# Kernel tuning notes

Hardware: AMD Instinct MI355X
Metric: run time of the kernel (lower is better)

Reference implementation:

```python
import jax, jax.numpy as jnp
import numpy as np

B, S, D = 1, 2048, 1024          # batch, seq, n_embd
E, F = 16, 1024                  # n_routed_experts, moe_intermediate_size
NG, TKG, K = 4, 2, 4             # n_group, topk_group, num_experts_per_tok
NSH = 2                          # n_shared_experts
SCALE = 2.5                      # routed_scaling_factor
STD = 0.02
EPG = E // NG                    # experts per group


def setup_inputs() -> dict:
    key = jax.random.key(0)
    ks = jax.random.split(key, 8)
    return {
        "hidden_states": jax.random.normal(ks[0], (B, S, D), jnp.float32),
        "router_w": jax.random.normal(ks[1], (E, D), jnp.float32) * STD,   # gate.weight
        "bias": jnp.zeros((E,), jnp.float32),                              # e_score_correction_bias
        "gate_w": jax.random.normal(ks[2], (E, D, F), jnp.float32) * STD,  # per-expert gate_proj (transposed)
        "up_w": jax.random.normal(ks[3], (E, D, F), jnp.float32) * STD,    # per-expert up_proj
        "down_w": jax.random.normal(ks[4], (E, F, D), jnp.float32) * STD,  # per-expert down_proj
        "sh_gate_w": jax.random.normal(ks[5], (D, NSH * F), jnp.float32) * STD,
        "sh_up_w": jax.random.normal(ks[6], (D, NSH * F), jnp.float32) * STD,
        "sh_down_w": jax.random.normal(ks[7], (NSH * F, D), jnp.float32) * STD,
    }


def _route(x_flat, router_w, bias):
    # x_flat: [T, D] -> topk_idx [T, K], topk_w [T, K]
    logits = x_flat.astype(jnp.float32) @ router_w.T          # [T, E]
    scores = jax.nn.sigmoid(logits)
    s = scores + bias[None, :]                                # scores_for_choice
    sg = s.reshape(-1, NG, EPG)
    group_score = jax.lax.top_k(sg, 2)[0].sum(-1)             # sum of top-2 per group [T, NG]
    gidx = jax.lax.top_k(group_score, TKG)[1]                 # [T, TKG]
    gmask = jnp.sum(jax.nn.one_hot(gidx, NG, dtype=jnp.float32), axis=1) > 0   # [T, NG]
    emask = jnp.repeat(gmask, EPG, axis=1)                    # [T, E]
    masked = jnp.where(emask, s, -1.0)
    topk_idx = jax.lax.top_k(masked, K)[1]                    # [T, K]
    tw = jnp.take_along_axis(scores, topk_idx, axis=1)        # gather raw sigmoid scores
    tw = tw / (tw.sum(-1, keepdims=True) + 1e-20)             # norm_topk_prob
    tw = tw * SCALE
    return topk_idx, tw


def reference(hidden_states, router_w, bias, gate_w, up_w, down_w,
              sh_gate_w, sh_up_w, sh_down_w):
    x = hidden_states.reshape(-1, D)                          # [T, D]
    topk_idx, tw = _route(x, router_w, bias)
    # combine weights per (token, expert): scatter-add of topk weights
    combine = (jax.nn.one_hot(topk_idx, E, dtype=tw.dtype) * tw[..., None]).sum(1)  # [T, E]
    # per-expert SwiGLU MLPs (dense dispatch, masked combine == index_add semantics)
    h = jnp.einsum('td,edf->etf', x, gate_w)                  # [E, T, F]
    u = jnp.einsum('td,edf->etf', x, up_w)
    y = jnp.einsum('etf,efd->etd', jax.nn.silu(h) * u, down_w)  # [E, T, D]
    routed = jnp.einsum('etd,te->td', y, combine)             # weighted combine
    # shared experts
    sh = (jax.nn.silu(x @ sh_gate_w) * (x @ sh_up_w)) @ sh_down_w
    return (routed + sh).reshape(hidden_states.shape)
```

## Files before the change

kernel.cpp:

```cpp
#include <hip/hip_runtime.h>
#include <cstdint>
#include <cstddef>


#define T_TOK 2048
#define DIM   1024
#define NEXP  16
#define MAXTILES 80
#define SH_TILES 32
#define GRID_Y (MAXTILES + SH_TILES)
#define NBLK (8 * GRID_Y)
#define ABASE_SH 10240

typedef __bf16 bf16x8_t __attribute__((ext_vector_type(8)));
typedef float  f32x4_t  __attribute__((ext_vector_type(4)));
typedef unsigned short ushort8_t __attribute__((ext_vector_type(8)));
typedef unsigned short ushort4_t __attribute__((ext_vector_type(4)));

#define OFF_XB     (0UL)
#define OFF_SHGT   (4UL<<20)
#define OFF_SHUT   (8UL<<20)
#define OFF_GATET  (12UL<<20)
#define OFF_UPT    (44UL<<20)
#define OFF_DOWNT  (76UL<<20)
#define OFF_SHDT   (108UL<<20)
#define OFF_ACT    (112UL<<20)
#define OFF_YSLOT  (140UL<<20)
#define OFF_PART   (0UL)
#define OFF_CTRL   (160UL<<20)
#define CT_OFFSETS  128
#define CT_NTILES   192
#define CT_TILEEXP  256
#define CT_SLOTTOK  4096
#define CT_TKSLOT   49152
#define CT_TOPKIDX  81920
#define CT_TOPKW    114688

__device__ __forceinline__ unsigned short f2bf(float f) {
  __bf16 h = (__bf16)f;
  return __builtin_bit_cast(unsigned short, h);
}
__device__ __forceinline__ float bf2f(unsigned short u) {
  unsigned int v = ((unsigned int)u) << 16;
  return __builtin_bit_cast(float, v);
}
__device__ __forceinline__ void gld16(const void* g, void* l) {
  __builtin_amdgcn_global_load_lds(
      (const __attribute__((address_space(1))) void*)(g),
      (__attribute__((address_space(3))) void*)(l), 16, 0, 0);
}

#define VWAIT6 asm volatile("s_waitcnt vmcnt(6)" ::: "memory")
#define VWAIT4 asm volatile("s_waitcnt vmcnt(4)" ::: "memory")
#define VWAIT0 asm volatile("s_waitcnt vmcnt(0)" ::: "memory")
#define BAR { __builtin_amdgcn_s_barrier(); __builtin_amdgcn_sched_barrier(0); }

__device__ __forceinline__ void tbody(const float* __restrict__ src,
                                      unsigned short* __restrict__ dst,
                                      int R, int C) {
  __shared__ unsigned short tile[128 * 132];
  int cT = blockIdx.x * 128, rT = blockIdx.y * 128;
  int t = threadIdx.x;
  int rb = t >> 5, cb = t & 31;
  float f[4][4][4];
#pragma unroll
  for (int p = 0; p < 4; p++)
#pragma unroll
    for (int i = 0; i < 4; i++) {
      float4 v = *(const float4*)(src + (long)(rT + p * 32 + 4 * rb + i) * C + cT + 4 * cb);
      f[p][i][0] = v.x; f[p][i][1] = v.y; f[p][i][2] = v.z; f[p][i][3] = v.w;
    }
#pragma unroll
  for (int p = 0; p < 4; p++)
#pragma unroll
    for (int j = 0; j < 4; j++) {
      ushort4_t o;
      o[0] = f2bf(f[p][0][j]); o[1] = f2bf(f[p][1][j]);
      o[2] = f2bf(f[p][2][j]); o[3] = f2bf(f[p][3][j]);
      *(ushort4_t*)&tile[(4 * cb + j) * 132 + p * 32 + 4 * rb] = o;
    }
  __syncthreads();
#pragma unroll
  for (int m = 0; m < 8; m++) {
    int q = t + 256 * m;
    int c = q >> 4, r0 = (q & 15) * 8;
    ushort4_t lo = *(const ushort4_t*)&tile[c * 132 + r0];
    ushort4_t hi = *(const ushort4_t*)&tile[c * 132 + r0 + 4];
    ushort8_t w8 = {lo[0], lo[1], lo[2], lo[3], hi[0], hi[1], hi[2], hi[3]};
    *(ushort8_t*)(dst + (long)(cT + c) * R + rT + r0) = w8;
  }
}

__global__ void k_transpose(const float* __restrict__ src, unsigned short* __restrict__ dst,
                            int R, int C) {
  long b = blockIdx.z;
  tbody(src + b * (long)R * C, dst + b * (long)R * C, R, C);
}

__global__ void k_transpose3(const float* __restrict__ g, const float* __restrict__ u,
                             const float* __restrict__ d, unsigned short* __restrict__ gT,
                             unsigned short* __restrict__ uT, unsigned short* __restrict__ dT) {
  int z = blockIdx.z;
  int which = z >> 4;
  long b = z & 15;
  const float* s = (which == 0) ? g : (which == 1) ? u : d;
  unsigned short* t = (which == 0) ? gT : (which == 1) ? uT : dT;
  tbody(s + b * 1048576L, t + b * 1048576L, 1024, 1024);
}

__global__ void k_transpose_sh(const float* __restrict__ sg, const float* __restrict__ su,
                               unsigned short* __restrict__ gT, unsigned short* __restrict__ uT) {
  const float* s = blockIdx.z ? su : sg;
  unsigned short* t = blockIdx.z ? uT : gT;
  tbody(s, t, 1024, 2048);
}

__global__ __launch_bounds__(256) void k_router(
    const float* __restrict__ x, const float* __restrict__ rw,
    const float* __restrict__ bias, int* __restrict__ topk_idx,
    float* __restrict__ topk_w, unsigned short* __restrict__ xb) {
  int t = blockIdx.x, tid = threadIdx.x;
  int wv = tid >> 6, lane = tid & 63;
  float4 xv = ((const float4*)(x + (size_t)t * DIM))[tid];
  ushort4_t xo;
  xo[0] = f2bf(xv.x); xo[1] = f2bf(xv.y); xo[2] = f2bf(xv.z); xo[3] = f2bf(xv.w);
  ((ushort4_t*)(xb + (size_t)t * DIM))[tid] = xo;
  float part[NEXP];
#pragma unroll
  for (int e = 0; e < NEXP; e++) {
    float4 wr = ((const float4*)(rw + (size_t)e * DIM))[tid];
    part[e] = xv.x * wr.x + xv.y * wr.y + xv.z * wr.z + xv.w * wr.w;
  }
  __shared__ float wsum_s[4 * NEXP];
#pragma unroll
  for (int e = 0; e < NEXP; e++) {
    float v = part[e];
#pragma unroll
    for (int off = 32; off; off >>= 1) v += __shfl_xor(v, off, 64);
    if (lane == 0) wsum_s[wv * NEXP + e] = v;
  }
  __syncthreads();
  if (tid == 0) {
    float r_sc[NEXP], r_s[NEXP];
#pragma unroll
    for (int e = 0; e < NEXP; e++) {
      float logit = wsum_s[e] + wsum_s[NEXP + e] + wsum_s[2 * NEXP + e] +
                    wsum_s[3 * NEXP + e];
      float sc = 1.f / (1.f + expf(-logit));
      r_sc[e] = sc;
      r_s[e] = sc + bias[e];
    }
    float gs[4];
#pragma unroll
    for (int g = 0; g < 4; g++) {
      float m1 = -1e30f, m2 = -1e30f;
#pragma unroll
      for (int j = 0; j < 4; j++) {
        float v = r_s[g * 4 + j];
        if (v > m1) { m2 = m1; m1 = v; } else if (v > m2) m2 = v;
      }
      gs[g] = m1 + m2;
    }
    int g1 = 0;
    for (int g = 1; g < 4; g++) if (gs[g] > gs[g1]) g1 = g;
    int g2 = -1;
    for (int g = 0; g < 4; g++) { if (g == g1) continue; if (g2 < 0 || gs[g] > gs[g2]) g2 = g; }
    int taken = 0, idx[4];
    float w[4], wsum = 1e-20f;
#pragma unroll
    for (int k = 0; k < 4; k++) {
      float best = -1e30f; int bi = 0;
#pragma unroll
      for (int e2 = 0; e2 < 16; e2++) {
        if (taken & (1 << e2)) continue;
        int g = e2 >> 2;
        float v = (g == g1 || g == g2) ? r_s[e2] : -1.f;
        if (v > best) { best = v; bi = e2; }
      }
      taken |= 1 << bi; idx[k] = bi;
    }
#pragma unroll
    for (int k = 0; k < 4; k++) { w[k] = r_sc[idx[k]]; wsum += w[k]; }
    float sc2 = 2.5f / wsum;
#pragma unroll
    for (int k = 0; k < 4; k++) {
      topk_idx[t * 4 + k] = idx[k];
      topk_w[t * 4 + k] = w[k] * sc2;
    }
  }
}

__global__ __launch_bounds__(256) void k_route_post(
    const int* __restrict__ topk_idx, int* __restrict__ offsets,
    int* __restrict__ tile_expert, int* __restrict__ n_tiles,
    int* __restrict__ slot_token, int* __restrict__ tk_slot) {
  __shared__ int cnt[NEXP][257];
  __shared__ int offs[NEXP], tot[NEXP];
  int tid = threadIdx.x;
  int4 ent[8];
#pragma unroll
  for (int i = 0; i < 8; i++) ent[i] = ((const int4*)topk_idx)[tid * 8 + i];
  int lc[NEXP];
#pragma unroll
  for (int j = 0; j < NEXP; j++) lc[j] = 0;
#pragma unroll
  for (int i = 0; i < 8; i++) {
    int es[4] = {ent[i].x, ent[i].y, ent[i].z, ent[i].w};
#pragma unroll
    for (int k = 0; k < 4; k++)
#pragma unroll
      for (int j = 0; j < NEXP; j++) lc[j] += (es[k] == j) ? 1 : 0;
  }
#pragma unroll
  for (int j = 0; j < NEXP; j++) cnt[j][tid] = lc[j];
  __syncthreads();
  if (tid < NEXP) {
    int base = 0;
    for (int c = 0; c < 256; c += 8) {
      int v[8];
#pragma unroll
      for (int i = 0; i < 8; i++) v[i] = cnt[tid][c + i];
#pragma unroll
      for (int i = 0; i < 8; i++) { cnt[tid][c + i] = base; base += v[i]; }
    }
    tot[tid] = base;
  }
  __syncthreads();
  if (tid == 0) {
    int cum = 0, tt = 0;
    for (int e = 0; e < NEXP; e++) {
      offs[e] = cum;
      offsets[e] = cum;
      int nt = (tot[e] + 127) >> 7;
      for (int i = 0; i < nt; i++) tile_expert[tt++] = e;
      cum += nt << 7;
    }
    n_tiles[0] = tt;
  }
  __syncthreads();
  for (int e = 0; e < NEXP; e++) {
    int s0 = offs[e] + tot[e];
    int s1 = offs[e] + (((tot[e] + 127) >> 7) << 7);
    for (int s = s0 + tid; s < s1; s += 256) slot_token[s] = -1;
  }
  int lcur[NEXP];
#pragma unroll
  for (int j = 0; j < NEXP; j++) lcur[j] = offs[j] + cnt[j][tid];
#pragma unroll
  for (int i = 0; i < 8; i++) {
    int t = tid * 8 + i;
    int es[4] = {ent[i].x, ent[i].y, ent[i].z, ent[i].w};
#pragma unroll
    for (int k = 0; k < 4; k++) {
      int e = es[k], pos = 0;
#pragma unroll
      for (int j = 0; j < NEXP; j++) pos += (e == j) ? lcur[j] : 0;
#pragma unroll
      for (int j = 0; j < NEXP; j++) lcur[j] += (e == j) ? 1 : 0;
      slot_token[pos] = t;
      tk_slot[t * 4 + k] = pos;
    }
  }
}

__global__ __launch_bounds__(256, 2) void k_gateup(
    const unsigned short* __restrict__ xb, const unsigned short* __restrict__ gateT,
    const unsigned short* __restrict__ upT, const unsigned short* __restrict__ shGT,
    const unsigned short* __restrict__ shUT, unsigned short* __restrict__ act,
    const int* __restrict__ slot_token, const int* __restrict__ tile_expert,
    const int* __restrict__ n_tiles) {
  int o = blockIdx.x;
  int wk = (o & 7) * GRID_Y + (o >> 3);
  int nx = wk & 7, bt = wk >> 3;
  int NT = n_tiles[0];
  bool routed = bt < NT;
  const unsigned short *Bg, *Bu;
  int actbase, tokbase = 0;
  if (routed) {
    int e = tile_expert[bt];
    Bg = gateT + ((size_t)e << 20);
    Bu = upT + ((size_t)e << 20);
    actbase = bt * 128;
  } else {
    int st = bt - NT;
    if (st >= SH_TILES) return;
    int se = st >> 4, tt = st & 15;
    Bg = shGT + ((size_t)se << 20);
    Bu = shUT + ((size_t)se << 20);
    actbase = ABASE_SH + se * T_TOK + tt * 128;
    tokbase = tt * 128;
  }
  int n0 = nx * 128;

  __shared__ unsigned short lds[3 * 3 * 128 * 32];

  int tid = threadIdx.x;
  int w = tid >> 6, L = tid & 63;
  int c0 = w * 128 + L, c1 = c0 + 64;
  int ar0 = c0 >> 2, ar1 = c1 >> 2;
  int ch0 = (c0 & 3) ^ (ar0 & 3), ch1 = (c1 & 3) ^ (ar1 & 3);
  long arow0, arow1;
  if (routed) {
    int t0 = slot_token[bt * 128 + ar0]; if (t0 < 0) t0 = 0;
    int t1 = slot_token[bt * 128 + ar1]; if (t1 < 0) t1 = 0;
    arow0 = t0; arow1 = t1;
  } else {
    arow0 = tokbase + ar0; arow1 = tokbase + ar1;
  }
  const char* aA = (const char*)(xb + arow0 * 1024) + ch0 * 16;
  const char* aB = (const char*)(xb + arow1 * 1024) + ch1 * 16;
  const char* gA = (const char*)(Bg + (size_t)(n0 + ar0) * 1024) + ch0 * 16;
  const char* gB = (const char*)(Bg + (size_t)(n0 + ar1) * 1024) + ch1 * 16;
  const char* uA = (const char*)(Bu + (size_t)(n0 + ar0) * 1024) + ch0 * 16;
  const char* uB = (const char*)(Bu + (size_t)(n0 + ar1) * 1024) + ch1 * 16;
  const int a0o = w * 2048, a1o = w * 2048 + 1024;
  const int g0o = 8192 + w * 2048, g1o = 8192 + w * 2048 + 1024;
  const int u0o = 16384 + w * 2048, u1o = 16384 + w * 2048 + 1024;

  f32x4_t accg[4][4], accu[4][4];
#pragma unroll
  for (int i = 0; i < 4; i++)
#pragma unroll
    for (int j = 0; j < 4; j++) {
      accg[i][j] = f32x4_t{0.f, 0.f, 0.f, 0.f};
      accu[i][j] = f32x4_t{0.f, 0.f, 0.f, 0.f};
    }

  int mb = (w >> 1) * 64, nb = (w & 1) * 64;
  int lr = L & 15, quad = L >> 4;
  int sw = ((quad ^ (lr & 3)) << 3);

#define GU_STAGE(BOFF)                                                       \
  { char* bp = (char*)lds + (BOFF);                                          \
    gld16(aA, bp + a0o); gld16(aB, bp + a1o);                                \
    gld16(gA, bp + g0o); gld16(gB, bp + g1o);                                \
    gld16(uA, bp + u0o); gld16(uB, bp + u1o);                                \
    aA += 64; aB += 64; gA += 64; gB += 64; uA += 64; uB += 64; }

#define GU_COMPUTE(UOFF)                                                     \
  { const unsigned short* pA = lds + (UOFF);                                 \
    const unsigned short* pG = pA + 4096;                                    \
    const unsigned short* pU = pA + 8192;                                    \
    bf16x8_t af[4], bg[4], bu[4];                                            \
    _Pragma("unroll")                                                        \
    for (int i = 0; i < 4; i++) af[i] = *(const bf16x8_t*)(pA + (mb + 16 * i + lr) * 32 + sw); \
    _Pragma("unroll")                                                        \
    for (int i = 0; i < 4; i++) bg[i] = *(const bf16x8_t*)(pG + (nb + 16 * i + lr) * 32 + sw); \
    _Pragma("unroll")                                                        \
    for (int i = 0; i < 4; i++) bu[i] = *(const bf16x8_t*)(pU + (nb + 16 * i + lr) * 32 + sw); \
    _Pragma("unroll")                                                        \
    for (int i = 0; i < 4; i++)                                              \
      _Pragma("unroll")                                                      \
      for (int j = 0; j < 4; j++) {                                          \
        accg[i][j] = __builtin_amdgcn_mfma_f32_16x16x32_bf16(af[i], bg[j], accg[i][j], 0, 0, 0); \
        accu[i][j] = __builtin_amdgcn_mfma_f32_16x16x32_bf16(af[i], bu[j], accu[i][j], 0, 0, 0); \
      } }

  GU_STAGE(0); GU_STAGE(24576);
#pragma unroll 1
  for (int p = 0; p < 10; ++p) {
    VWAIT6; BAR; GU_STAGE(49152); GU_COMPUTE(0);
    VWAIT6; BAR; GU_STAGE(0);     GU_COMPUTE(12288);
    VWAIT6; BAR; GU_STAGE(24576); GU_COMPUTE(24576);
  }
  VWAIT6; BAR; GU_COMPUTE(0);
  VWAIT0; BAR; GU_COMPUTE(12288);
#undef GU_STAGE
#undef GU_COMPUTE

#pragma unroll
  for (int i = 0; i < 4; i++) {
    int rowb = actbase + mb + 16 * i + quad * 4;
#pragma unroll
    for (int j = 0; j < 4; j++) {
      int col = n0 + nb + 16 * j + lr;
#pragma unroll
      for (int r = 0; r < 4; r++) {
        float h = accg[i][j][r];
        float u = accu[i][j][r];
        float a = h / (1.f + __expf(-h)) * u;
        act[(size_t)(rowb + r) * 1024 + col] = f2bf(a);
      }
    }
  }
}

__global__ __launch_bounds__(256, 2) void k_down(
    const unsigned short* __restrict__ act, const unsigned short* __restrict__ downT,
    const unsigned short* __restrict__ shDT, unsigned short* __restrict__ yslot,
    float* __restrict__ part, const int* __restrict__ tile_expert,
    const int* __restrict__ n_tiles) {
  int o = blockIdx.x;
  int wk = (o & 7) * GRID_Y + (o >> 3);
  int nx = wk & 7, bt = wk >> 3;
  int NT = n_tiles[0];
  bool routed = bt < NT;
  const unsigned short* B;
  size_t bstride;
  int abase, obase, se = 0;
  if (routed) {
    int e = tile_expert[bt];
    B = downT + ((size_t)e << 20);
    bstride = 1024;
    abase = bt * 128;
    obase = bt * 128;
  } else {
    int st = bt - NT;
    if (st >= SH_TILES) return;
    se = st >> 4;
    int tt = st & 15;
    B = shDT + se * 1024;
    bstride = 2048;
    abase = ABASE_SH + se * T_TOK + tt * 128;
    obase = tt * 128;
  }
  int n0 = nx * 128;

  __shared__ unsigned short lds[3 * 2 * 128 * 32];

  int tid = threadIdx.x;
  int w = tid >> 6, L = tid & 63;
  int c0 = w * 128 + L, c1 = c0 + 64;
  int ar0 = c0 >> 2, ar1 = c1 >> 2;
  int ch0 = (c0 & 3) ^ (ar0 & 3), ch1 = (c1 & 3) ^ (ar1 & 3);
  const char* aA = (const char*)(act + (size_t)(abase + ar0) * 1024) + ch0 * 16;
  const char* aB = (const char*)(act + (size_t)(abase + ar1) * 1024) + ch1 * 16;
  const char* bA = (const char*)(B + (size_t)(n0 + ar0) * bstride) + ch0 * 16;
  const char* bB = (const char*)(B + (size_t)(n0 + ar1) * bstride) + ch1 * 16;
  const int a0o = w * 2048, a1o = w * 2048 + 1024;
  const int b0o = 8192 + w * 2048, b1o = 8192 + w * 2048 + 1024;

  f32x4_t acc[4][4];
#pragma unroll
  for (int i = 0; i < 4; i++)
#pragma unroll
    for (int j = 0; j < 4; j++) acc[i][j] = f32x4_t{0.f, 0.f, 0.f, 0.f};

  int mb = (w >> 1) * 64, nb = (w & 1) * 64;
  int lr = L & 15, quad = L >> 4;
  int sw = ((quad ^ (lr & 3)) << 3);

#define DN_STAGE(BOFF)                                                       \
  { char* bp = (char*)lds + (BOFF);                                          \
    gld16(aA, bp + a0o); gld16(aB, bp + a1o);                                \
    gld16(bA, bp + b0o); gld16(bB, bp + b1o);                                \
    aA += 64; aB += 64; bA += 64; bB += 64; }

#define DN_COMPUTE(UOFF)                                                     \
  { const unsigned short* pA = lds + (UOFF);                                 \
    const unsigned short* pB = pA + 4096;                                    \
    bf16x8_t af[4], bb[4];                                                   \
    _Pragma("unroll")                                                        \
    for (int i = 0; i < 4; i++) af[i] = *(const bf16x8_t*)(pA + (mb + 16 * i + lr) * 32 + sw); \
    _Pragma("unroll")                                                        \
    for (int i = 0; i < 4; i++) bb[i] = *(const bf16x8_t*)(pB + (nb + 16 * i + lr) * 32 + sw); \
    _Pragma("unroll")                                                        \
    for (int i = 0; i < 4; i++)                                              \
      _Pragma("unroll")                                                      \
      for (int j = 0; j < 4; j++)                                            \
        acc[i][j] = __builtin_amdgcn_mfma_f32_16x16x32_bf16(af[i], bb[j], acc[i][j], 0, 0, 0); }

  DN_STAGE(0); DN_STAGE(16384);
#pragma unroll 1
  for (int p = 0; p < 10; ++p) {
    VWAIT4; BAR; DN_STAGE(32768); DN_COMPUTE(0);
    VWAIT4; BAR; DN_STAGE(0);     DN_COMPUTE(8192);
    VWAIT4; BAR; DN_STAGE(16384); DN_COMPUTE(16384);
  }
  VWAIT4; BAR; DN_COMPUTE(0);
  VWAIT0; BAR; DN_COMPUTE(8192);
#undef DN_STAGE
#undef DN_COMPUTE

#pragma unroll
  for (int i = 0; i < 4; i++) {
    int rowb = obase + mb + 16 * i + quad * 4;
#pragma unroll
    for (int j = 0; j < 4; j++) {
      int col = n0 + nb + 16 * j + lr;
#pragma unroll
      for (int r = 0; r < 4; r++) {
        float v = acc[i][j][r];
        if (routed) yslot[(size_t)(rowb + r) * 1024 + col] = f2bf(v);
        else part[(size_t)se * (T_TOK * 1024) + (size_t)(rowb + r) * 1024 + col] = v;
      }
    }
  }
}

__global__ void k_gather(float* __restrict__ out, const float* __restrict__ partial,
                         const unsigned short* __restrict__ yslot,
                         const int* __restrict__ tk_slot, const float* __restrict__ topk_w) {
  int t = blockIdx.x, tid = threadIdx.x;
  int4 sl = ((const int4*)tk_slot)[t];
  float4 wv = ((const float4*)topk_w)[t];
  int d = 4 * tid;
  float4 p0 = *(const float4*)(partial + (size_t)t * 1024 + d);
  float4 p1 = *(const float4*)(partial + (size_t)(T_TOK * 1024) + (size_t)t * 1024 + d);
  float4 o = {p0.x + p1.x, p0.y + p1.y, p0.z + p1.z, p0.w + p1.w};
  const int s[4] = {sl.x, sl.y, sl.z, sl.w};
  const float wk[4] = {wv.x, wv.y, wv.z, wv.w};
#pragma unroll
  for (int k = 0; k < 4; k++) {
    ushort4_t y = *(const ushort4_t*)(yslot + (size_t)s[k] * 1024 + d);
    o.x += wk[k] * bf2f(y[0]);
    o.y += wk[k] * bf2f(y[1]);
    o.z += wk[k] * bf2f(y[2]);
    o.w += wk[k] * bf2f(y[3]);
  }
  *(float4*)(out + (size_t)t * 1024 + d) = o;
}

extern "C" void kernel_launch(void* const* d_in, const int* in_sizes, int n_in,
                              void* d_out, int out_size, void* d_ws, size_t ws_size,
                              hipStream_t stream) {
  const float* x = (const float*)d_in[0];
  const float* rw = (const float*)d_in[1];
  const float* bias = (const float*)d_in[2];
  const float* gw = (const float*)d_in[3];
  const float* uw = (const float*)d_in[4];
  const float* dw = (const float*)d_in[5];
  const float* sg = (const float*)d_in[6];
  const float* su = (const float*)d_in[7];
  const float* sd = (const float*)d_in[8];
  float* out = (float*)d_out;
  char* ws = (char*)d_ws;

  unsigned short* xb    = (unsigned short*)(ws + OFF_XB);
  unsigned short* shGT  = (unsigned short*)(ws + OFF_SHGT);
  unsigned short* shUT  = (unsigned short*)(ws + OFF_SHUT);
  unsigned short* gateT = (unsigned short*)(ws + OFF_GATET);
  unsigned short* upT   = (unsigned short*)(ws + OFF_UPT);
  unsigned short* downT = (unsigned short*)(ws + OFF_DOWNT);
  unsigned short* shDT  = (unsigned short*)(ws + OFF_SHDT);
  unsigned short* act   = (unsigned short*)(ws + OFF_ACT);
  unsigned short* yslot = (unsigned short*)(ws + OFF_YSLOT);
  float*          part  = (float*)(ws + OFF_PART);
  char* ctrl = ws + OFF_CTRL;
  int* offsets_    = (int*)(ctrl + CT_OFFSETS);
  int* n_tiles     = (int*)(ctrl + CT_NTILES);
  int* tile_expert = (int*)(ctrl + CT_TILEEXP);
  int* slot_token  = (int*)(ctrl + CT_SLOTTOK);
  int* tk_slot     = (int*)(ctrl + CT_TKSLOT);
  int* topk_idx    = (int*)(ctrl + CT_TOPKIDX);
  float* topk_w    = (float*)(ctrl + CT_TOPKW);

  k_transpose3<<<dim3(8, 8, 48), 256, 0, stream>>>(gw, uw, dw, gateT, upT, downT);
  k_transpose_sh<<<dim3(16, 8, 2), 256, 0, stream>>>(sg, su, shGT, shUT);
  k_transpose<<<dim3(8, 16, 1), 256, 0, stream>>>(sd, shDT, 2048, 1024);
  k_router<<<2048, 256, 0, stream>>>(x, rw, bias, topk_idx, topk_w, xb);
  k_route_post<<<1, 256, 0, stream>>>(topk_idx, offsets_, tile_expert, n_tiles,
                                      slot_token, tk_slot);
  k_gateup<<<NBLK, 256, 0, stream>>>(xb, gateT, upT, shGT, shUT, act,
                                     slot_token, tile_expert, n_tiles);
  k_down<<<NBLK, 256, 0, stream>>>(act, downT, shDT, yslot, part,
                                   tile_expert, n_tiles);
  k_gather<<<2048, 256, 0, stream>>>(out, part, yslot, tk_slot, topk_w);
}
```

Before: 418.8 us.

## Halve N tile to 64, double-buffer LDS, raise occupancy in MoE GEMMs

Shrinks the N tile of the gate/up and down GEMM kernels from 128 to 64 columns and doubles the grid, switching from a 3-stage to a 2-stage LDS buffer. This raises occupancy from 2 to 4 blocks per CU and improves load balance across the expert tiles. The MFMA block is wrapped in s_setprio to favour math waves. In exchange, each block re-reads its A (activation) tile for half as many columns, adding global traffic, and the extra barrier per stage shortens prefetch overlap.

New measurement: 432.8 us. 1.03x slower.

```diff
diff --git a/kernel.cpp b/kernel.cpp
--- a/kernel.cpp
+++ b/kernel.cpp
@@ -9,7 +9,7 @@
 #define MAXTILES 80
 #define SH_TILES 32
 #define GRID_Y (MAXTILES + SH_TILES)
-#define NBLK (8 * GRID_Y)
+#define NBLK2 (16 * GRID_Y)
 #define ABASE_SH 10240
 
 typedef __bf16 bf16x8_t __attribute__((ext_vector_type(8)));
@@ -50,8 +50,8 @@
       (__attribute__((address_space(3))) void*)(l), 16, 0, 0);
 }
 
-#define VWAIT6 asm volatile("s_waitcnt vmcnt(6)" ::: "memory")
 #define VWAIT4 asm volatile("s_waitcnt vmcnt(4)" ::: "memory")
+#define VWAIT3 asm volatile("s_waitcnt vmcnt(3)" ::: "memory")
 #define VWAIT0 asm volatile("s_waitcnt vmcnt(0)" ::: "memory")
 #define BAR { __builtin_amdgcn_s_barrier(); __builtin_amdgcn_sched_barrier(0); }
 
@@ -263,15 +263,15 @@
   }
 }
 
-__global__ __launch_bounds__(256, 2) void k_gateup(
+__global__ __launch_bounds__(256, 4) void k_gateup(
     const unsigned short* __restrict__ xb, const unsigned short* __restrict__ gateT,
     const unsigned short* __restrict__ upT, const unsigned short* __restrict__ shGT,
     const unsigned short* __restrict__ shUT, unsigned short* __restrict__ act,
     const int* __restrict__ slot_token, const int* __restrict__ tile_expert,
     const int* __restrict__ n_tiles) {
   int o = blockIdx.x;
-  int wk = (o & 7) * GRID_Y + (o >> 3);
-  int nx = wk & 7, bt = wk >> 3;
+  int wk = (o & 7) * (2 * GRID_Y) + (o >> 3);
+  int nx = wk & 15, bt = wk >> 4;
   int NT = n_tiles[0];
   bool routed = bt < NT;
   const unsigned short *Bg, *Bu;
@@ -290,9 +290,9 @@
     actbase = ABASE_SH + se * T_TOK + tt * 128;
     tokbase = tt * 128;
   }
-  int n0 = nx * 128;
-
-  __shared__ unsigned short lds[3 * 3 * 128 * 32];
+  int n0 = nx * 64;
+
+  __shared__ unsigned short lds[2 * 8192];
 
   int tid = threadIdx.x;
   int w = tid >> 6, L = tid & 63;
@@ -307,64 +307,64 @@
   } else {
     arow0 = tokbase + ar0; arow1 = tokbase + ar1;
   }
+  int arb = tid >> 2;
+  int chb = (tid & 3) ^ (arb & 3);
   const char* aA = (const char*)(xb + arow0 * 1024) + ch0 * 16;
   const char* aB = (const char*)(xb + arow1 * 1024) + ch1 * 16;
-  const char* gA = (const char*)(Bg + (size_t)(n0 + ar0) * 1024) + ch0 * 16;
-  const char* gB = (const char*)(Bg + (size_t)(n0 + ar1) * 1024) + ch1 * 16;
-  const char* uA = (const char*)(Bu + (size_t)(n0 + ar0) * 1024) + ch0 * 16;
-  const char* uB = (const char*)(Bu + (size_t)(n0 + ar1) * 1024) + ch1 * 16;
+  const char* gA = (const char*)(Bg + (size_t)(n0 + arb) * 1024) + chb * 16;
+  const char* uA = (const char*)(Bu + (size_t)(n0 + arb) * 1024) + chb * 16;
   const int a0o = w * 2048, a1o = w * 2048 + 1024;
-  const int g0o = 8192 + w * 2048, g1o = 8192 + w * 2048 + 1024;
-  const int u0o = 16384 + w * 2048, u1o = 16384 + w * 2048 + 1024;
-
-  f32x4_t accg[4][4], accu[4][4];
+  const int gBo = 8192 + w * 1024;
+  const int uBo = 12288 + w * 1024;
+
+  f32x4_t accg[4][2], accu[4][2];
 #pragma unroll
   for (int i = 0; i < 4; i++)
 #pragma unroll
-    for (int j = 0; j < 4; j++) {
+    for (int j = 0; j < 2; j++) {
       accg[i][j] = f32x4_t{0.f, 0.f, 0.f, 0.f};
       accu[i][j] = f32x4_t{0.f, 0.f, 0.f, 0.f};
     }
 
-  int mb = (w >> 1) * 64, nb = (w & 1) * 64;
+  int mb = (w >> 1) * 64, nb = (w & 1) * 32;
   int lr = L & 15, quad = L >> 4;
   int sw = ((quad ^ (lr & 3)) << 3);
 
 #define GU_STAGE(BOFF)                                                       \
   { char* bp = (char*)lds + (BOFF);                                          \
     gld16(aA, bp + a0o); gld16(aB, bp + a1o);                                \
-    gld16(gA, bp + g0o); gld16(gB, bp + g1o);                                \
-    gld16(uA, bp + u0o); gld16(uB, bp + u1o);                                \
-    aA += 64; aB += 64; gA += 64; gB += 64; uA += 64; uB += 64; }
+    gld16(gA, bp + gBo); gld16(uA, bp + uBo);                                \
+    aA += 64; aB += 64; gA += 64; uA += 64; }
 
 #define GU_COMPUTE(UOFF)                                                     \
   { const unsigned short* pA = lds + (UOFF);                                 \
     const unsigned short* pG = pA + 4096;                                    \
-    const unsigned short* pU = pA + 8192;                                    \
-    bf16x8_t af[4], bg[4], bu[4];                                            \
+    const unsigned short* pU = pA + 6144;                                    \
+    bf16x8_t af[4], bg[2], bu[2];                                            \
     _Pragma("unroll")                                                        \
     for (int i = 0; i < 4; i++) af[i] = *(const bf16x8_t*)(pA + (mb + 16 * i + lr) * 32 + sw); \
     _Pragma("unroll")                                                        \
-    for (int i = 0; i < 4; i++) bg[i] = *(const bf16x8_t*)(pG + (nb + 16 * i + lr) * 32 + sw); \
-    _Pragma("unroll")                                                        \
-    for (int i = 0; i < 4; i++) bu[i] = *(const bf16x8_t*)(pU + (nb + 16 * i + lr) * 32 + sw); \
+    for (int j = 0; j < 2; j++) bg[j] = *(const bf16x8_t*)(pG + (nb + 16 * j + lr) * 32 + sw); \
+    _Pragma("unroll")                                                        \
+    for (int j = 0; j < 2; j++) bu[j] = *(const bf16x8_t*)(pU + (nb + 16 * j + lr) * 32 + sw); \
+    __builtin_amdgcn_s_setprio(1);                                           \
     _Pragma("unroll")                                                        \
     for (int i = 0; i < 4; i++)                                              \
       _Pragma("unroll")                                                      \
-      for (int j = 0; j < 4; j++) {                                          \
+      for (int j = 0; j < 2; j++) {                                          \
         accg[i][j] = __builtin_amdgcn_mfma_f32_16x16x32_bf16(af[i], bg[j], accg[i][j], 0, 0, 0); \
         accu[i][j] = __builtin_amdgcn_mfma_f32_16x16x32_bf16(af[i], bu[j], accu[i][j], 0, 0, 0); \
-      } }
-
-  GU_STAGE(0); GU_STAGE(24576);
+      }                                                                      \
+    __builtin_amdgcn_s_setprio(0); }
+
+  GU_STAGE(0); GU_STAGE(16384);
 #pragma unroll 1
-  for (int p = 0; p < 10; ++p) {
-    VWAIT6; BAR; GU_STAGE(49152); GU_COMPUTE(0);
-    VWAIT6; BAR; GU_STAGE(0);     GU_COMPUTE(12288);
-    VWAIT6; BAR; GU_STAGE(24576); GU_COMPUTE(24576);
-  }
-  VWAIT6; BAR; GU_COMPUTE(0);
-  VWAIT0; BAR; GU_COMPUTE(12288);
+  for (int p = 0; p < 15; ++p) {
+    VWAIT4; BAR; GU_COMPUTE(0);    BAR; GU_STAGE(0);
+    VWAIT4; BAR; GU_COMPUTE(8192); BAR; GU_STAGE(16384);
+  }
+  VWAIT4; BAR; GU_COMPUTE(0);
+  VWAIT0; BAR; GU_COMPUTE(8192);
 #undef GU_STAGE
 #undef GU_COMPUTE
 
@@ -372,7 +372,7 @@
   for (int i = 0; i < 4; i++) {
     int rowb = actbase + mb + 16 * i + quad * 4;
 #pragma unroll
-    for (int j = 0; j < 4; j++) {
+    for (int j = 0; j < 2; j++) {
       int col = n0 + nb + 16 * j + lr;
 #pragma unroll
       for (int r = 0; r < 4; r++) {
@@ -385,14 +385,14 @@
   }
 }
 
-__global__ __launch_bounds__(256, 2) void k_down(
+__global__ __launch_bounds__(256, 4) void k_down(
     const unsigned short* __restrict__ act, const unsigned short* __restrict__ downT,
     const unsigned short* __restrict__ shDT, unsigned short* __restrict__ yslot,
     float* __restrict__ part, const int* __restrict__ tile_expert,
     const int* __restrict__ n_tiles) {
   int o = blockIdx.x;
-  int wk = (o & 7) * GRID_Y + (o >> 3);
-  int nx = wk & 7, bt = wk >> 3;
+  int wk = (o & 7) * (2 * GRID_Y) + (o >> 3);
+  int nx = wk & 15, bt = wk >> 4;
   int NT = n_tiles[0];
   bool routed = bt < NT;
   const unsigned short* B;
@@ -414,61 +414,63 @@
     abase = ABASE_SH + se * T_TOK + tt * 128;
     obase = tt * 128;
   }
-  int n0 = nx * 128;
-
-  __shared__ unsigned short lds[3 * 2 * 128 * 32];
+  int n0 = nx * 64;
+
+  __shared__ unsigned short lds[2 * 6144];
 
   int tid = threadIdx.x;
   int w = tid >> 6, L = tid & 63;
   int c0 = w * 128 + L, c1 = c0 + 64;
   int ar0 = c0 >> 2, ar1 = c1 >> 2;
   int ch0 = (c0 & 3) ^ (ar0 & 3), ch1 = (c1 & 3) ^ (ar1 & 3);
+  int arb = tid >> 2;
+  int chb = (tid & 3) ^ (arb & 3);
   const char* aA = (const char*)(act + (size_t)(abase + ar0) * 1024) + ch0 * 16;
   const char* aB = (const char*)(act + (size_t)(abase + ar1) * 1024) + ch1 * 16;
-  const char* bA = (const char*)(B + (size_t)(n0 + ar0) * bstride) + ch0 * 16;
-  const char* bB = (const char*)(B + (size_t)(n0 + ar1) * bstride) + ch1 * 16;
+  const char* bA = (const char*)(B + (size_t)(n0 + arb) * bstride) + chb * 16;
   const int a0o = w * 2048, a1o = w * 2048 + 1024;
-  const int b0o = 8192 + w * 2048, b1o = 8192 + w * 2048 + 1024;
-
-  f32x4_t acc[4][4];
+  const int bBo = 8192 + w * 1024;
+
+  f32x4_t acc[4][2];
 #pragma unroll
   for (int i = 0; i < 4; i++)
 #pragma unroll
-    for (int j = 0; j < 4; j++) acc[i][j] = f32x4_t{0.f, 0.f, 0.f, 0.f};
-
-  int mb = (w >> 1) * 64, nb = (w & 1) * 64;
+    for (int j = 0; j < 2; j++) acc[i][j] = f32x4_t{0.f, 0.f, 0.f, 0.f};
+
+  int mb = (w >> 1) * 64, nb = (w & 1) * 32;
   int lr = L & 15, quad = L >> 4;
   int sw = ((quad ^ (lr & 3)) << 3);
 
 #define DN_STAGE(BOFF)                                                       \
   { char* bp = (char*)lds + (BOFF);                                          \
     gld16(aA, bp + a0o); gld16(aB, bp + a1o);                                \
-    gld16(bA, bp + b0o); gld16(bB, bp + b1o);                                \
-    aA += 64; aB += 64; bA += 64; bB += 64; }
+    gld16(bA, bp + bBo);                                                     \
+    aA += 64; aB += 64; bA += 64; }
 
 #define DN_COMPUTE(UOFF)                                                     \
   { const unsigned short* pA = lds + (UOFF);                                 \
     const unsigned short* pB = pA + 4096;                                    \
-    bf16x8_t af[4], bb[4];                                                   \
+    bf16x8_t af[4], bb[2];                                                   \
     _Pragma("unroll")                                                        \
     for (int i = 0; i < 4; i++) af[i] = *(const bf16x8_t*)(pA + (mb + 16 * i + lr) * 32 + sw); \
     _Pragma("unroll")                                                        \
-    for (int i = 0; i < 4; i++) bb[i] = *(const bf16x8_t*)(pB + (nb + 16 * i + lr) * 32 + sw); \
+    for (int j = 0; j < 2; j++) bb[j] = *(const bf16x8_t*)(pB + (nb + 16 * j + lr) * 32 + sw); \
+    __builtin_amdgcn_s_setprio(1);                                           \
     _Pragma("unroll")                                                        \
     for (int i = 0; i < 4; i++)                                              \
       _Pragma("unroll")                                                      \
-      for (int j = 0; j < 4; j++)                                            \
-        acc[i][j] = __builtin_amdgcn_mfma_f32_16x16x32_bf16(af[i], bb[j], acc[i][j], 0, 0, 0); }
-
-  DN_STAGE(0); DN_STAGE(16384);
+      for (int j = 0; j < 2; j++)                                            \
+        acc[i][j] = __builtin_amdgcn_mfma_f32_16x16x32_bf16(af[i], bb[j], acc[i][j], 0, 0, 0); \
+    __builtin_amdgcn_s_setprio(0); }
+
+  DN_STAGE(0); DN_STAGE(12288);
 #pragma unroll 1
-  for (int p = 0; p < 10; ++p) {
-    VWAIT4; BAR; DN_STAGE(32768); DN_COMPUTE(0);
-    VWAIT4; BAR; DN_STAGE(0);     DN_COMPUTE(8192);
-    VWAIT4; BAR; DN_STAGE(16384); DN_COMPUTE(16384);
-  }
-  VWAIT4; BAR; DN_COMPUTE(0);
-  VWAIT0; BAR; DN_COMPUTE(8192);
+  for (int p = 0; p < 15; ++p) {
+    VWAIT3; BAR; DN_COMPUTE(0);    BAR; DN_STAGE(0);
+    VWAIT3; BAR; DN_COMPUTE(6144); BAR; DN_STAGE(12288);
+  }
+  VWAIT3; BAR; DN_COMPUTE(0);
+  VWAIT0; BAR; DN_COMPUTE(6144);
 #undef DN_STAGE
 #undef DN_COMPUTE
 
@@ -476,7 +478,7 @@
   for (int i = 0; i < 4; i++) {
     int rowb = obase + mb + 16 * i + quad * 4;
 #pragma unroll
-    for (int j = 0; j < 4; j++) {
+    for (int j = 0; j < 2; j++) {
       int col = n0 + nb + 16 * j + lr;
 #pragma unroll
       for (int r = 0; r < 4; r++) {
@@ -551,9 +553,9 @@
   k_router<<<2048, 256, 0, stream>>>(x, rw, bias, topk_idx, topk_w, xb);
   k_route_post<<<1, 256, 0, stream>>>(topk_idx, offsets_, tile_expert, n_tiles,
                                       slot_token, tk_slot);
-  k_gateup<<<NBLK, 256, 0, stream>>>(xb, gateT, upT, shGT, shUT, act,
-                                     slot_token, tile_expert, n_tiles);
-  k_down<<<NBLK, 256, 0, stream>>>(act, downT, shDT, yslot, part,
-                                   tile_expert, n_tiles);
+  k_gateup<<<NBLK2, 256, 0, stream>>>(xb, gateT, upT, shGT, shUT, act,
+                                      slot_token, tile_expert, n_tiles);
+  k_down<<<NBLK2, 256, 0, stream>>>(act, downT, shDT, yslot, part,
+                                    tile_expert, n_tiles);
   k_gather<<<2048, 256, 0, stream>>>(out, part, yslot, tk_slot, topk_w);
 }
```
